# Performance work log

Hardware: AMD Instinct MI355X
Metric: run time of the kernel (lower is better)

## Reference

```python
import jax, jax.numpy as jnp
import numpy as np

# SoftmaxMatMulSparse forward: out = softmax(x1, dim=-1) @ x2.
# The masker/sparsify/quantize path only compresses activations saved for
# backward; the forward output is the exact dense softmax-matmul.

def setup_inputs() -> dict:
    key = jax.random.key(0)
    k1, k2 = jax.random.split(key)
    x1 = jax.random.normal(k1, (1, 16, 2048, 2048), dtype=jnp.float32)  # [B,H,S,S] scores
    x2 = jax.random.normal(k2, (1, 16, 2048, 64), dtype=jnp.float32)    # [B,H,S,Dh] values
    return {"x1": x1, "x2": x2}

def reference(x1, x2):
    probs = jax.nn.softmax(x1, axis=-1)          # [B,H,S,S]
    return jnp.matmul(probs, x2)                 # [B,H,S,Dh]
```

## Files before the change

kernel.cpp:

```cpp
#include <hip/hip_runtime.h>
#include <hip/hip_bf16.h>
#include <stdint.h>


#define H_  16
#define S_  2048
#define D_  64
#define KT  128
#define QT  64

typedef short bf16x8 __attribute__((ext_vector_type(8)));
typedef float f32x4  __attribute__((ext_vector_type(4)));

__device__ __forceinline__ uint16_t f2bf(float f) {
  uint32_t u = __builtin_bit_cast(uint32_t, f);
  u += 0x7fffu + ((u >> 16) & 1u);
  return (uint16_t)(u >> 16);
}

__global__ __launch_bounds__(256) void vtrans_kernel(const float* __restrict__ x2,
                                                     uint16_t* __restrict__ x2t) {
  __shared__ float t[D_][64 + 1];
  const int h  = blockIdx.x >> 5;
  const int k0 = (blockIdx.x & 31) << 6;
  const float* src = x2 + ((size_t)h * S_ + k0) * D_;
#pragma unroll
  for (int p = 0; p < 4; ++p) {
    int flat = p * 1024 + threadIdx.x * 4;
    int k = flat >> 6, d = flat & 63;
    float4 v = *(const float4*)(src + (size_t)k * D_ + d);
    t[d + 0][k] = v.x; t[d + 1][k] = v.y; t[d + 2][k] = v.z; t[d + 3][k] = v.w;
  }
  __syncthreads();
  uint16_t* dst = x2t + (size_t)h * D_ * S_ + k0;
#pragma unroll
  for (int p = 0; p < 4; ++p) {
    int flat = p * 1024 + threadIdx.x * 4;
    int d = flat >> 6, k = flat & 63;
    ushort4 o;
    o.x = f2bf(t[d][k + 0]); o.y = f2bf(t[d][k + 1]);
    o.z = f2bf(t[d][k + 2]); o.w = f2bf(t[d][k + 3]);
    *(ushort4*)(dst + (size_t)d * S_ + k) = o;
  }
}

__global__ __launch_bounds__(256) void smm_kernel(const float* __restrict__ x1,
                                                  const float* __restrict__ x2,
                                                  const uint16_t* __restrict__ x2t,
                                                  int use_t,
                                                  float* __restrict__ out) {
  __shared__ __attribute__((aligned(16))) uint16_t pT[QT][KT];
  __shared__ __attribute__((aligned(16))) uint16_t vT[D_][KT];

  const int tid  = threadIdx.x;
  const int lane = tid & 63;
  const int w    = tid >> 6;
  const int h    = blockIdx.x >> 5;
  const int q0   = (blockIdx.x & 31) * QT;

  f32x4 acc[4];
  f32x4 accS;
#pragma unroll
  for (int c = 0; c < 4; ++c) acc[c] = (f32x4){0.f, 0.f, 0.f, 0.f};
  accS = (f32x4){0.f, 0.f, 0.f, 0.f};

  bf16x8 ones;
  {
    short v = ((lane & 15) == 0) ? (short)0x3F80 : (short)0;
#pragma unroll
    for (int e = 0; e < 8; ++e) ones[e] = v;
  }

  const float* x1p = x1 + ((size_t)h * S_ + q0) * S_;
  const int prow = tid >> 5;
  const int pk4  = (tid & 31) << 2;
  const int arow = lane & 15;
  const int kgrp = lane >> 4;

  for (int kt = 0; kt < S_ / KT; ++kt) {
    __syncthreads();

#pragma unroll
    for (int p = 0; p < 8; ++p) {
      int r = prow + p * 8;
      float4 v = *(const float4*)(x1p + (size_t)r * S_ + kt * KT + pk4);
      uint32_t lo = (uint32_t)f2bf(__expf(v.x)) | ((uint32_t)f2bf(__expf(v.y)) << 16);
      uint32_t hi = (uint32_t)f2bf(__expf(v.z)) | ((uint32_t)f2bf(__expf(v.w)) << 16);
      int byteoff = (pk4 * 2) ^ ((r & 15) << 4);
      *(uint2*)((char*)(&pT[r][0]) + byteoff) = make_uint2(lo, hi);
    }

    if (use_t) {
      const uint16_t* vp = x2t + (size_t)h * D_ * S_ + kt * KT;
#pragma unroll
      for (int p = 0; p < 4; ++p) {
        int flat = p * 256 + tid;
        int dd = flat >> 4;
        int ch = flat & 15;
        uint4 v = *(const uint4*)(vp + (size_t)dd * S_ + ch * 8);
        int byteoff = (ch * 16) ^ ((dd & 15) << 4);
        *(uint4*)((char*)(&vT[dd][0]) + byteoff) = v;
      }
    } else {
      int dd = tid & 63;
      int kg = tid >> 6;
      const float* src = x2 + ((size_t)h * S_ + kt * KT) * D_ + dd;
#pragma unroll
      for (int p = 0; p < 4; ++p) {
        int kb = p * 32 + kg * 8;
        uint16_t tmp[8];
#pragma unroll
        for (int j = 0; j < 8; ++j) tmp[j] = f2bf(src[(size_t)(kb + j) * D_]);
        int byteoff = (kb * 2) ^ ((dd & 15) << 4);
        *(uint4*)((char*)(&vT[dd][0]) + byteoff) = *(uint4*)tmp;
      }
    }
    __syncthreads();

#pragma unroll
    for (int ks = 0; ks < 4; ++ks) {
      int kb = ks * 64 + kgrp * 16;
      int ar = w * 16 + arow;
      bf16x8 a = *(const bf16x8*)((const char*)(&pT[ar][0]) + (kb ^ (arow << 4)));
      accS = __builtin_amdgcn_mfma_f32_16x16x32_bf16(a, ones, accS, 0, 0, 0);
#pragma unroll
      for (int c = 0; c < 4; ++c) {
        int bc = c * 16 + arow;
        bf16x8 b = *(const bf16x8*)((const char*)(&vT[bc][0]) + (kb ^ (arow << 4)));
        acc[c] = __builtin_amdgcn_mfma_f32_16x16x32_bf16(a, b, acc[c], 0, 0, 0);
      }
    }
  }

  float* op = out + ((size_t)h * S_ + q0 + w * 16) * D_;
#pragma unroll
  for (int j = 0; j < 4; ++j) {
    float s = __shfl(accS[j], lane & 48);
    float rs = 1.0f / s;
    int row = (lane >> 4) * 4 + j;
#pragma unroll
    for (int c = 0; c < 4; ++c) {
      op[(size_t)row * D_ + c * 16 + (lane & 15)] = acc[c][j] * rs;
    }
  }
}

extern "C" void kernel_launch(void* const* d_in, const int* in_sizes, int n_in,
                              void* d_out, int out_size, void* d_ws, size_t ws_size,
                              hipStream_t stream) {
  const float* x1 = (const float*)d_in[0];
  const float* x2 = (const float*)d_in[1];
  float* out      = (float*)d_out;
  uint16_t* x2t   = (uint16_t*)d_ws;

  const size_t need = (size_t)H_ * D_ * S_ * sizeof(uint16_t);
  int use_t = (ws_size >= need) ? 1 : 0;

  if (use_t) {
    vtrans_kernel<<<dim3(H_ * (S_ / 64)), dim3(256), 0, stream>>>(x2, x2t);
  }
  smm_kernel<<<dim3(H_ * (S_ / QT)), dim3(256), 0, stream>>>(x1, x2, x2t, use_t, out);
}
```

Before: 64.36 us.

## Double-buffer LDS tiles and prefetch next tile into registers during MFMA

Splits the K-loop into load, write and MFMA phases with two LDS buffers. The global loads for the next tile are issued before the MFMAs on the current tile, so memory latency overlaps compute, and one barrier per iteration is dropped. It also adds nontemporal loads for x1 and nontemporal stores for the output to reduce cache pollution. The cost is doubled LDS (64KB) and more registers held across the loop, which may lower occupancy.

```diff
diff --git a/kernel.cpp b/kernel.cpp
--- a/kernel.cpp
+++ b/kernel.cpp
@@ -8,6 +8,7 @@
 #define D_  64
 #define KT  128
 #define QT  64
+#define NT  (S_ / KT)
 
 typedef short bf16x8 __attribute__((ext_vector_type(8)));
 typedef float f32x4  __attribute__((ext_vector_type(4)));
@@ -49,8 +50,8 @@
                                                   const uint16_t* __restrict__ x2t,
                                                   int use_t,
                                                   float* __restrict__ out) {
-  __shared__ __attribute__((aligned(16))) uint16_t pT[QT][KT];
-  __shared__ __attribute__((aligned(16))) uint16_t vT[D_][KT];
+  __shared__ __attribute__((aligned(16))) uint16_t pT[2][QT][KT];
+  __shared__ __attribute__((aligned(16))) uint16_t vT[2][D_][KT];
 
   const int tid  = threadIdx.x;
   const int lane = tid & 63;
@@ -77,19 +78,16 @@
   const int arow = lane & 15;
   const int kgrp = lane >> 4;
 
-  for (int kt = 0; kt < S_ / KT; ++kt) {
-    __syncthreads();
-
+  f32x4 x1v[8];
+  uint4  vtv[4];
+
+  auto load_tile = [&](int kt) {
 #pragma unroll
     for (int p = 0; p < 8; ++p) {
       int r = prow + p * 8;
-      float4 v = *(const float4*)(x1p + (size_t)r * S_ + kt * KT + pk4);
-      uint32_t lo = (uint32_t)f2bf(__expf(v.x)) | ((uint32_t)f2bf(__expf(v.y)) << 16);
-      uint32_t hi = (uint32_t)f2bf(__expf(v.z)) | ((uint32_t)f2bf(__expf(v.w)) << 16);
-      int byteoff = (pk4 * 2) ^ ((r & 15) << 4);
-      *(uint2*)((char*)(&pT[r][0]) + byteoff) = make_uint2(lo, hi);
-    }
-
+      const f32x4* src = (const f32x4*)(x1p + (size_t)r * S_ + kt * KT + pk4);
+      x1v[p] = __builtin_nontemporal_load(src);
+    }
     if (use_t) {
       const uint16_t* vp = x2t + (size_t)h * D_ * S_ + kt * KT;
 #pragma unroll
@@ -97,9 +95,7 @@
         int flat = p * 256 + tid;
         int dd = flat >> 4;
         int ch = flat & 15;
-        uint4 v = *(const uint4*)(vp + (size_t)dd * S_ + ch * 8);
-        int byteoff = (ch * 16) ^ ((dd & 15) << 4);
-        *(uint4*)((char*)(&vT[dd][0]) + byteoff) = v;
+        vtv[p] = *(const uint4*)(vp + (size_t)dd * S_ + ch * 8);
       }
     } else {
       int dd = tid & 63;
@@ -111,25 +107,67 @@
         uint16_t tmp[8];
 #pragma unroll
         for (int j = 0; j < 8; ++j) tmp[j] = f2bf(src[(size_t)(kb + j) * D_]);
+        vtv[p] = *(uint4*)tmp;
+      }
+    }
+  };
+
+  auto write_tile = [&](int buf) {
+#pragma unroll
+    for (int p = 0; p < 8; ++p) {
+      int r = prow + p * 8;
+      f32x4 v = x1v[p];
+      uint32_t lo = (uint32_t)f2bf(__expf(v[0])) | ((uint32_t)f2bf(__expf(v[1])) << 16);
+      uint32_t hi = (uint32_t)f2bf(__expf(v[2])) | ((uint32_t)f2bf(__expf(v[3])) << 16);
+      int byteoff = (pk4 * 2) ^ ((r & 15) << 4);
+      *(uint2*)((char*)(&pT[buf][r][0]) + byteoff) = make_uint2(lo, hi);
+    }
+    if (use_t) {
+#pragma unroll
+      for (int p = 0; p < 4; ++p) {
+        int flat = p * 256 + tid;
+        int dd = flat >> 4;
+        int ch = flat & 15;
+        int byteoff = (ch * 16) ^ ((dd & 15) << 4);
+        *(uint4*)((char*)(&vT[buf][dd][0]) + byteoff) = vtv[p];
+      }
+    } else {
+      int dd = tid & 63;
+      int kg = tid >> 6;
+#pragma unroll
+      for (int p = 0; p < 4; ++p) {
+        int kb = p * 32 + kg * 8;
         int byteoff = (kb * 2) ^ ((dd & 15) << 4);
-        *(uint4*)((char*)(&vT[dd][0]) + byteoff) = *(uint4*)tmp;
-      }
-    }
-    __syncthreads();
-
+        *(uint4*)((char*)(&vT[buf][dd][0]) + byteoff) = vtv[p];
+      }
+    }
+  };
+
+  auto mfma_tile = [&](int buf) {
 #pragma unroll
     for (int ks = 0; ks < 4; ++ks) {
       int kb = ks * 64 + kgrp * 16;
       int ar = w * 16 + arow;
-      bf16x8 a = *(const bf16x8*)((const char*)(&pT[ar][0]) + (kb ^ (arow << 4)));
+      bf16x8 a = *(const bf16x8*)((const char*)(&pT[buf][ar][0]) + (kb ^ (arow << 4)));
       accS = __builtin_amdgcn_mfma_f32_16x16x32_bf16(a, ones, accS, 0, 0, 0);
 #pragma unroll
       for (int c = 0; c < 4; ++c) {
         int bc = c * 16 + arow;
-        bf16x8 b = *(const bf16x8*)((const char*)(&vT[bc][0]) + (kb ^ (arow << 4)));
+        bf16x8 b = *(const bf16x8*)((const char*)(&vT[buf][bc][0]) + (kb ^ (arow << 4)));
         acc[c] = __builtin_amdgcn_mfma_f32_16x16x32_bf16(a, b, acc[c], 0, 0, 0);
       }
     }
+  };
+
+  load_tile(0);
+  write_tile(0);
+  int cur = 0;
+  for (int kt = 0; kt < NT; ++kt) {
+    __syncthreads();
+    if (kt + 1 < NT) load_tile(kt + 1);
+    mfma_tile(cur);
+    if (kt + 1 < NT) write_tile(cur ^ 1);
+    cur ^= 1;
   }
 
   float* op = out + ((size_t)h * S_ + q0 + w * 16) * D_;
@@ -140,7 +178,8 @@
     int row = (lane >> 4) * 4 + j;
 #pragma unroll
     for (int c = 0; c < 4; ++c) {
-      op[(size_t)row * D_ + c * 16 + (lane & 15)] = acc[c][j] * rs;
+      float o = acc[c][j] * rs;
+      __builtin_nontemporal_store(o, op + (size_t)row * D_ + c * 16 + (lane & 15));
     }
   }
 }
```

Measured after the change: 64.52 us. No clear change (+0.3%).

## Replace LDS-staged softmax-matmul with direct register-fed MFMA kernel

Applied to the files above, without the earlier changes.

Adds a kernel in which each wave loads its rows of x1 straight from global memory into MFMA operand registers, using nontemporal loads laid out to match the MFMA fragment. B fragments come directly from the pre-transposed bf16 V. This removes shared-memory staging, both __syncthreads per tile, and the ones-vector MFMA used for row sums, which are now computed in FP32 with shuffles. Output stores are nontemporal. The cost is that the four waves no longer share V through LDS, so each wave re-reads V from global memory/cache, and there is no software double-buffering to hide load latency.

```diff
diff --git a/kernel.cpp b/kernel.cpp
--- a/kernel.cpp
+++ b/kernel.cpp
@@ -6,8 +6,8 @@
 #define H_  16
 #define S_  2048
 #define D_  64
-#define KT  128
 #define QT  64
+#define NT  (S_ / 128)
 
 typedef short bf16x8 __attribute__((ext_vector_type(8)));
 typedef float f32x4  __attribute__((ext_vector_type(4)));
@@ -44,13 +44,77 @@
   }
 }
 
-__global__ __launch_bounds__(256) void smm_kernel(const float* __restrict__ x1,
-                                                  const float* __restrict__ x2,
+__global__ __launch_bounds__(256) void smm_direct(const float* __restrict__ x1,
                                                   const uint16_t* __restrict__ x2t,
-                                                  int use_t,
                                                   float* __restrict__ out) {
-  __shared__ __attribute__((aligned(16))) uint16_t pT[QT][KT];
-  __shared__ __attribute__((aligned(16))) uint16_t vT[D_][KT];
+  const int tid  = threadIdx.x;
+  const int lane = tid & 63;
+  const int w    = tid >> 6;
+  const int h    = blockIdx.x >> 5;
+  const int q0   = (blockIdx.x & 31) * QT + w * 16;
+  const int arow = lane & 15;
+  const int kgrp = lane >> 4;
+
+  const float* ap = x1 + ((size_t)(h * S_ + q0 + arow)) * S_ + kgrp * 8;
+  const uint16_t* bbase = x2t + (size_t)h * D_ * S_ + (size_t)arow * S_ + kgrp * 8;
+  const uint16_t* b0p = bbase;
+  const uint16_t* b1p = bbase + (size_t)16 * S_;
+  const uint16_t* b2p = bbase + (size_t)32 * S_;
+  const uint16_t* b3p = bbase + (size_t)48 * S_;
+
+  f32x4 acc[4];
+#pragma unroll
+  for (int c = 0; c < 4; ++c) acc[c] = (f32x4){0.f, 0.f, 0.f, 0.f};
+  float rsum = 0.f;
+
+#pragma unroll 4
+  for (int kt = 0; kt < S_ / 32; ++kt) {
+    const int k0 = kt * 32;
+    f32x4 a0 = __builtin_nontemporal_load((const f32x4*)(ap + k0));
+    f32x4 a1 = __builtin_nontemporal_load((const f32x4*)(ap + k0 + 4));
+    uint4 b0 = *(const uint4*)(b0p + k0);
+    uint4 b1 = *(const uint4*)(b1p + k0);
+    uint4 b2 = *(const uint4*)(b2p + k0);
+    uint4 b3 = *(const uint4*)(b3p + k0);
+
+    float e0 = __expf(a0[0]), e1 = __expf(a0[1]), e2 = __expf(a0[2]), e3 = __expf(a0[3]);
+    float e4 = __expf(a1[0]), e5 = __expf(a1[1]), e6 = __expf(a1[2]), e7 = __expf(a1[3]);
+    rsum += ((e0 + e1) + (e2 + e3)) + ((e4 + e5) + (e6 + e7));
+
+    bf16x8 af;
+    af[0] = (short)f2bf(e0); af[1] = (short)f2bf(e1);
+    af[2] = (short)f2bf(e2); af[3] = (short)f2bf(e3);
+    af[4] = (short)f2bf(e4); af[5] = (short)f2bf(e5);
+    af[6] = (short)f2bf(e6); af[7] = (short)f2bf(e7);
+
+    acc[0] = __builtin_amdgcn_mfma_f32_16x16x32_bf16(af, __builtin_bit_cast(bf16x8, b0), acc[0], 0, 0, 0);
+    acc[1] = __builtin_amdgcn_mfma_f32_16x16x32_bf16(af, __builtin_bit_cast(bf16x8, b1), acc[1], 0, 0, 0);
+    acc[2] = __builtin_amdgcn_mfma_f32_16x16x32_bf16(af, __builtin_bit_cast(bf16x8, b2), acc[2], 0, 0, 0);
+    acc[3] = __builtin_amdgcn_mfma_f32_16x16x32_bf16(af, __builtin_bit_cast(bf16x8, b3), acc[3], 0, 0, 0);
+  }
+
+  rsum += __shfl_xor(rsum, 16);
+  rsum += __shfl_xor(rsum, 32);
+
+  float* op = out + ((size_t)(h * S_ + q0)) * D_;
+#pragma unroll
+  for (int j = 0; j < 4; ++j) {
+    int row = (lane >> 4) * 4 + j;
+    float s = __shfl(rsum, row);
+    float rs = 1.0f / s;
+#pragma unroll
+    for (int c = 0; c < 4; ++c) {
+      float o = acc[c][j] * rs;
+      __builtin_nontemporal_store(o, op + (size_t)row * D_ + c * 16 + arow);
+    }
+  }
+}
+
+__global__ __launch_bounds__(256) void smm_lds(const float* __restrict__ x1,
+                                               const float* __restrict__ x2,
+                                               float* __restrict__ out) {
+  __shared__ __attribute__((aligned(16))) uint16_t pT[QT][128];
+  __shared__ __attribute__((aligned(16))) uint16_t vT[D_][128];
 
   const int tid  = threadIdx.x;
   const int lane = tid & 63;
@@ -77,34 +141,21 @@
   const int arow = lane & 15;
   const int kgrp = lane >> 4;
 
-  for (int kt = 0; kt < S_ / KT; ++kt) {
+  for (int kt = 0; kt < NT; ++kt) {
     __syncthreads();
-
 #pragma unroll
     for (int p = 0; p < 8; ++p) {
       int r = prow + p * 8;
-      float4 v = *(const float4*)(x1p + (size_t)r * S_ + kt * KT + pk4);
+      float4 v = *(const float4*)(x1p + (size_t)r * S_ + kt * 128 + pk4);
       uint32_t lo = (uint32_t)f2bf(__expf(v.x)) | ((uint32_t)f2bf(__expf(v.y)) << 16);
       uint32_t hi = (uint32_t)f2bf(__expf(v.z)) | ((uint32_t)f2bf(__expf(v.w)) << 16);
       int byteoff = (pk4 * 2) ^ ((r & 15) << 4);
       *(uint2*)((char*)(&pT[r][0]) + byteoff) = make_uint2(lo, hi);
     }
-
-    if (use_t) {
-      const uint16_t* vp = x2t + (size_t)h * D_ * S_ + kt * KT;
-#pragma unroll
-      for (int p = 0; p < 4; ++p) {
-        int flat = p * 256 + tid;
-        int dd = flat >> 4;
-        int ch = flat & 15;
-        uint4 v = *(const uint4*)(vp + (size_t)dd * S_ + ch * 8);
-        int byteoff = (ch * 16) ^ ((dd & 15) << 4);
-        *(uint4*)((char*)(&vT[dd][0]) + byteoff) = v;
-      }
-    } else {
+    {
       int dd = tid & 63;
       int kg = tid >> 6;
-      const float* src = x2 + ((size_t)h * S_ + kt * KT) * D_ + dd;
+      const float* src = x2 + ((size_t)h * S_ + kt * 128) * D_ + dd;
 #pragma unroll
       for (int p = 0; p < 4; ++p) {
         int kb = p * 32 + kg * 8;
@@ -116,7 +167,6 @@
       }
     }
     __syncthreads();
-
 #pragma unroll
     for (int ks = 0; ks < 4; ++ks) {
       int kb = ks * 64 + kgrp * 16;
@@ -154,10 +204,10 @@
   uint16_t* x2t   = (uint16_t*)d_ws;
 
   const size_t need = (size_t)H_ * D_ * S_ * sizeof(uint16_t);
-  int use_t = (ws_size >= need) ? 1 : 0;
-
-  if (use_t) {
+  if (ws_size >= need) {
     vtrans_kernel<<<dim3(H_ * (S_ / 64)), dim3(256), 0, stream>>>(x2, x2t);
-  }
-  smm_kernel<<<dim3(H_ * (S_ / QT)), dim3(256), 0, stream>>>(x1, x2, x2t, use_t, out);
-}
+    smm_direct<<<dim3(H_ * (S_ / QT)), dim3(256), 0, stream>>>(x1, x2t, out);
+  } else {
+    smm_lds<<<dim3(H_ * (S_ / QT)), dim3(256), 0, stream>>>(x1, x2, out);
+  }
+}
```

Result: slower. 113.1 us (+75.7%).

## Add high-occupancy 16-row softmax-matmul kernel reading V fragments directly from global

Applied to the files above, without the earlier changes.

Adds a new main kernel that processes 16 query rows per 128-thread block, giving many more small blocks for higher occupancy. V fragments are loaded straight from the transposed bf16 workspace into registers instead of being staged in LDS. Row sums are now accumulated in fp32 from the exponentials rather than computed with a ones-vector MFMA. X1 loads and output stores use nontemporal hints, and block IDs are swizzled across heads. Each 16-row block re-reads the full V for its head, so L2 traffic for V grows, in exchange for less LDS and fewer MFMAs per tile.

```diff
diff --git a/kernel.cpp b/kernel.cpp
--- a/kernel.cpp
+++ b/kernel.cpp
@@ -6,8 +6,9 @@
 #define H_  16
 #define S_  2048
 #define D_  64
-#define KT  128
 #define QT  64
+#define QT2 16
+#define NT  (S_ / 128)
 
 typedef short bf16x8 __attribute__((ext_vector_type(8)));
 typedef float f32x4  __attribute__((ext_vector_type(4)));
@@ -44,13 +45,96 @@
   }
 }
 
-__global__ __launch_bounds__(256) void smm_kernel(const float* __restrict__ x1,
-                                                  const float* __restrict__ x2,
-                                                  const uint16_t* __restrict__ x2t,
-                                                  int use_t,
-                                                  float* __restrict__ out) {
-  __shared__ __attribute__((aligned(16))) uint16_t pT[QT][KT];
-  __shared__ __attribute__((aligned(16))) uint16_t vT[D_][KT];
+__global__ __launch_bounds__(128, 4) void smm_hiocc(const float* __restrict__ x1,
+                                                    const uint16_t* __restrict__ x2t,
+                                                    float* __restrict__ out) {
+  __shared__ __attribute__((aligned(16))) uint16_t pT[QT2][128];
+  __shared__ float rsum_lds[QT2];
+
+  const int bid  = (blockIdx.x & 7) * 256 + (blockIdx.x >> 3);
+  const int tid  = threadIdx.x;
+  const int lane = tid & 63;
+  const int w    = tid >> 6;
+  const int h    = bid >> 7;
+  const int q0   = (bid & 127) * QT2;
+
+  const int r16  = lane & 15;
+  const int kg   = lane >> 4;
+
+  const int srow = tid >> 3;
+  const int sseg = tid & 7;
+  const float* ap = x1 + ((size_t)(h * S_ + q0 + srow)) * S_ + sseg * 4;
+
+  const uint16_t* bb  = x2t + (size_t)h * D_ * S_ + (size_t)(w * 32 + r16) * S_ + kg * 8;
+  const uint16_t* b1b = bb + (size_t)16 * S_;
+
+  f32x4 acc0 = (f32x4){0.f, 0.f, 0.f, 0.f};
+  f32x4 acc1 = (f32x4){0.f, 0.f, 0.f, 0.f};
+  float rsum = 0.f;
+
+  for (int kt = 0; kt < 16; ++kt) {
+    const int kbase = kt * 128;
+
+    f32x4 a0 = __builtin_nontemporal_load((const f32x4*)(ap + kbase));
+    f32x4 a1 = __builtin_nontemporal_load((const f32x4*)(ap + kbase + 32));
+    f32x4 a2 = __builtin_nontemporal_load((const f32x4*)(ap + kbase + 64));
+    f32x4 a3 = __builtin_nontemporal_load((const f32x4*)(ap + kbase + 96));
+    uint4 bv0[4], bv1[4];
+#pragma unroll
+    for (int ks = 0; ks < 4; ++ks) {
+      bv0[ks] = *(const uint4*)(bb  + kbase + ks * 32);
+      bv1[ks] = *(const uint4*)(b1b + kbase + ks * 32);
+    }
+
+    {
+      f32x4 av[4] = {a0, a1, a2, a3};
+#pragma unroll
+      for (int p = 0; p < 4; ++p) {
+        float e0 = __expf(av[p][0]), e1 = __expf(av[p][1]);
+        float e2 = __expf(av[p][2]), e3 = __expf(av[p][3]);
+        rsum += (e0 + e1) + (e2 + e3);
+        uint32_t lo = (uint32_t)f2bf(e0) | ((uint32_t)f2bf(e1) << 16);
+        uint32_t hi = (uint32_t)f2bf(e2) | ((uint32_t)f2bf(e3) << 16);
+        int k = sseg * 4 + p * 32;
+        int byteoff = (k * 2) ^ ((srow & 15) << 4);
+        *(uint2*)((char*)(&pT[srow][0]) + byteoff) = make_uint2(lo, hi);
+      }
+    }
+    __syncthreads();
+
+#pragma unroll
+    for (int ks = 0; ks < 4; ++ks) {
+      int kb = ks * 64 + kg * 16;
+      bf16x8 af = *(const bf16x8*)((const char*)(&pT[r16][0]) + (kb ^ (r16 << 4)));
+      acc0 = __builtin_amdgcn_mfma_f32_16x16x32_bf16(af, __builtin_bit_cast(bf16x8, bv0[ks]), acc0, 0, 0, 0);
+      acc1 = __builtin_amdgcn_mfma_f32_16x16x32_bf16(af, __builtin_bit_cast(bf16x8, bv1[ks]), acc1, 0, 0, 0);
+    }
+    __syncthreads();
+  }
+
+  rsum += __shfl_xor(rsum, 1);
+  rsum += __shfl_xor(rsum, 2);
+  rsum += __shfl_xor(rsum, 4);
+  if ((lane & 7) == 0) rsum_lds[srow] = rsum;
+  __syncthreads();
+
+  float* op = out + ((size_t)(h * S_ + q0)) * D_;
+#pragma unroll
+  for (int j = 0; j < 4; ++j) {
+    int row = kg * 4 + j;
+    float rs = 1.0f / rsum_lds[row];
+    float o0 = acc0[j] * rs;
+    float o1 = acc1[j] * rs;
+    __builtin_nontemporal_store(o0, op + (size_t)row * D_ + w * 32 + r16);
+    __builtin_nontemporal_store(o1, op + (size_t)row * D_ + w * 32 + 16 + r16);
+  }
+}
+
+__global__ __launch_bounds__(256) void smm_lds(const float* __restrict__ x1,
+                                               const float* __restrict__ x2,
+                                               float* __restrict__ out) {
+  __shared__ __attribute__((aligned(16))) uint16_t pT[QT][128];
+  __shared__ __attribute__((aligned(16))) uint16_t vT[D_][128];
 
   const int tid  = threadIdx.x;
   const int lane = tid & 63;
@@ -77,37 +161,24 @@
   const int arow = lane & 15;
   const int kgrp = lane >> 4;
 
-  for (int kt = 0; kt < S_ / KT; ++kt) {
-    __syncthreads();
-
+  for (int kt = 0; kt < NT; ++kt) {
+    __syncthreads();
 #pragma unroll
     for (int p = 0; p < 8; ++p) {
       int r = prow + p * 8;
-      float4 v = *(const float4*)(x1p + (size_t)r * S_ + kt * KT + pk4);
+      float4 v = *(const float4*)(x1p + (size_t)r * S_ + kt * 128 + pk4);
       uint32_t lo = (uint32_t)f2bf(__expf(v.x)) | ((uint32_t)f2bf(__expf(v.y)) << 16);
       uint32_t hi = (uint32_t)f2bf(__expf(v.z)) | ((uint32_t)f2bf(__expf(v.w)) << 16);
       int byteoff = (pk4 * 2) ^ ((r & 15) << 4);
       *(uint2*)((char*)(&pT[r][0]) + byteoff) = make_uint2(lo, hi);
     }
-
-    if (use_t) {
-      const uint16_t* vp = x2t + (size_t)h * D_ * S_ + kt * KT;
+    {
+      int dd = tid & 63;
+      int kgq = tid >> 6;
+      const float* src = x2 + ((size_t)h * S_ + kt * 128) * D_ + dd;
 #pragma unroll
       for (int p = 0; p < 4; ++p) {
-        int flat = p * 256 + tid;
-        int dd = flat >> 4;
-        int ch = flat & 15;
-        uint4 v = *(const uint4*)(vp + (size_t)dd * S_ + ch * 8);
-        int byteoff = (ch * 16) ^ ((dd & 15) << 4);
-        *(uint4*)((char*)(&vT[dd][0]) + byteoff) = v;
-      }
-    } else {
-      int dd = tid & 63;
-      int kg = tid >> 6;
-      const float* src = x2 + ((size_t)h * S_ + kt * KT) * D_ + dd;
-#pragma unroll
-      for (int p = 0; p < 4; ++p) {
-        int kb = p * 32 + kg * 8;
+        int kb = p * 32 + kgq * 8;
         uint16_t tmp[8];
 #pragma unroll
         for (int j = 0; j < 8; ++j) tmp[j] = f2bf(src[(size_t)(kb + j) * D_]);
@@ -116,7 +187,6 @@
       }
     }
     __syncthreads();
-
 #pragma unroll
     for (int ks = 0; ks < 4; ++ks) {
       int kb = ks * 64 + kgrp * 16;
@@ -154,10 +224,10 @@
   uint16_t* x2t   = (uint16_t*)d_ws;
 
   const size_t need = (size_t)H_ * D_ * S_ * sizeof(uint16_t);
-  int use_t = (ws_size >= need) ? 1 : 0;
-
-  if (use_t) {
+  if (ws_size >= need) {
     vtrans_kernel<<<dim3(H_ * (S_ / 64)), dim3(256), 0, stream>>>(x2, x2t);
-  }
-  smm_kernel<<<dim3(H_ * (S_ / QT)), dim3(256), 0, stream>>>(x1, x2, x2t, use_t, out);
-}
+    smm_hiocc<<<dim3(H_ * (S_ / QT2)), dim3(128), 0, stream>>>(x1, x2t, out);
+  } else {
+    smm_lds<<<dim3(H_ * (S_ / QT)), dim3(256), 0, stream>>>(x1, x2, out);
+  }
+}
```

Result: slower. 84.33 us (+31.0%).
